# Performance work log

Measured on AMD Instinct MI355X. Metric: run time of the kernel, lower is better.

The kernel has to match this reference:

```python
import jax, jax.numpy as jnp
import numpy as np

B, T, C, FREQ = 32, 512, 22, 192
HID = 128


def setup_inputs() -> dict:
    key = jax.random.key(0)
    k1, k2, k3, k4, k5, k6 = jax.random.split(key, 6)
    x = jax.random.normal(k1, (B, T, C, FREQ), dtype=jnp.float32)
    A = jax.random.uniform(k2, (B, T, C, C), dtype=jnp.float32)
    # Linear weights (torch layout: [out, in]); scaled like torch default init
    W0 = jax.random.normal(k3, (HID, FREQ), dtype=jnp.float32) / np.sqrt(FREQ)
    b0 = jax.random.normal(k4, (HID,), dtype=jnp.float32) * 0.01
    W1 = jax.random.normal(k5, (HID, HID), dtype=jnp.float32) / np.sqrt(HID)
    b1 = jax.random.normal(k6, (HID,), dtype=jnp.float32) * 0.01
    return {"x": x, "A": A, "W0": W0, "b0": b0, "W1": W1, "b1": b1}


def reference(x, A, W0, b0, W1, b1):
    # Vectorized over B and T simultaneously (original python-loops over t).
    # Layer i: xt = relu(Linear(bmm(A_t, xt)))
    h = x  # [B,T,C,Freq]
    for W, b in ((W0, b0), (W1, b1)):
        h = jnp.einsum('btij,btjf->btif', A, h)          # adjacency mix over nodes
        h = jax.nn.relu(jnp.einsum('btcf,hf->btch', h, W) + b)  # Linear + ReLU
    # stack over t is implicit; mean over node dim C -> [B,T,HID]
    return h.mean(axis=2)
```

## Files before the change

kernel.cpp:

```cpp
#include <hip/hip_runtime.h>

#define CC 22
#define FF 192
#define HH 128
#define NBT (32 * 512)

typedef __attribute__((ext_vector_type(8))) __bf16 bf16x8;
typedef __attribute__((ext_vector_type(8))) short s16x8;
typedef __attribute__((ext_vector_type(4))) float f32x4;

__device__ __forceinline__ float bf2f(unsigned short u) {
    union { unsigned int i; float f; } v;
    v.i = ((unsigned int)u) << 16;
    return v.f;
}

__device__ __forceinline__ unsigned short f2bf(float f) {
    union { float f; unsigned int i; } v;
    v.f = f;
    return (unsigned short)((v.i + 0x7fffu + ((v.i >> 16) & 1u)) >> 16);
}

__device__ __forceinline__ void split2(float v, unsigned short& h, unsigned short& l) {
    h = f2bf(v);
    float r = v - bf2f(h);
    l = f2bf(r);
}

__device__ __forceinline__ bf16x8 bzero8() {
    s16x8 z = {0, 0, 0, 0, 0, 0, 0, 0};
    return __builtin_bit_cast(bf16x8, z);
}

__device__ __forceinline__ int inputs_are_bf16(const unsigned short* __restrict__ A,
                                               int tid) {
    const float v = bf2f(A[tid & 63]);
    return __all(v >= 0.0f && v <= 1.0001f);
}

#define WS0H 0
#define WS0L 24576
#define WS1H 49152
#define WS1L 65536

__global__ void convert_weights(const float* __restrict__ W0g,
                                const float* __restrict__ W1g,
                                const unsigned short* __restrict__ Aany,
                                unsigned short* __restrict__ wsW) {
    if (inputs_are_bf16(Aany, threadIdx.x)) return;
    const int i = blockIdx.x * 256 + threadIdx.x;
    if (i < HH * FF) {
        unsigned short h, l;
        split2(W0g[i], h, l);
        wsW[WS0H + i] = h;
        wsW[WS0L + i] = l;
    } else {
        const int j = i - HH * FF;
        if (j < HH * HH) {
            unsigned short h, l;
            split2(W1g[j], h, l);
            wsW[WS1H + j] = h;
            wsW[WS1L + j] = l;
        }
    }
}

__device__ void run_block_f32(
    const float* __restrict__ xg, const float* __restrict__ Ag,
    const float* __restrict__ W0g, const float* __restrict__ b0g,
    const float* __restrict__ W1g, const float* __restrict__ b1g,
    float* __restrict__ outg, int bt, int tid,
    float* sA, float* sX, float* sH1)
{
    float* sH2  = sX;
    float* sH3  = sH1;
    float* sRed = sA;

    const float* Ap = Ag + (size_t)bt * (CC * CC);
    for (int i = tid; i < CC * CC; i += 256) sA[i] = Ap[i];
    const float4* xp = (const float4*)(xg + (size_t)bt * (CC * FF));
    for (int i = tid; i < CC * FF / 4; i += 256) ((float4*)sX)[i] = xp[i];
    __syncthreads();

    for (int idx4 = tid; idx4 < CC * FF / 4; idx4 += 256) {
        const int c  = idx4 / (FF / 4);
        const int fq = idx4 - c * (FF / 4);
        float4 acc = make_float4(0.f, 0.f, 0.f, 0.f);
        #pragma unroll
        for (int j = 0; j < CC; ++j) {
            const float  a  = sA[c * CC + j];
            const float4 xv = *(const float4*)&sX[j * FF + 4 * fq];
            acc.x += a * xv.x; acc.y += a * xv.y;
            acc.z += a * xv.z; acc.w += a * xv.w;
        }
        ((float4*)sH1)[idx4] = acc;
    }
    __syncthreads();

    const int h  = tid & 127;
    const int ty = tid >> 7;

    {
        float acc[11];
        const float bb = b0g[h];
        #pragma unroll
        for (int i = 0; i < 11; ++i) acc[i] = bb;
        #pragma unroll 4
        for (int fq = 0; fq < FF / 4; ++fq) {
            float4 u = ((const float4*)(W0g + h * FF))[fq];
            #pragma unroll
            for (int i = 0; i < 11; ++i) {
                const float4 xv = *(const float4*)&sH1[(2 * i + ty) * FF + 4 * fq];
                acc[i] = fmaf(xv.x, u.x, fmaf(xv.y, u.y, fmaf(xv.z, u.z, fmaf(xv.w, u.w, acc[i]))));
            }
        }
        #pragma unroll
        for (int i = 0; i < 11; ++i)
            sH2[(2 * i + ty) * HH + h] = fmaxf(acc[i], 0.f);
    }
    __syncthreads();

    for (int idx4 = tid; idx4 < CC * HH / 4; idx4 += 256) {
        const int c  = idx4 / (HH / 4);
        const int kq = idx4 - c * (HH / 4);
        float4 acc = make_float4(0.f, 0.f, 0.f, 0.f);
        #pragma unroll
        for (int j = 0; j < CC; ++j) {
            const float  a  = sA[c * CC + j];
            const float4 xv = *(const float4*)&sH2[j * HH + 4 * kq];
            acc.x += a * xv.x; acc.y += a * xv.y;
            acc.z += a * xv.z; acc.w += a * xv.w;
        }
        ((float4*)sH3)[idx4] = acc;
    }
    __syncthreads();

    {
        float acc[11];
        const float bb = b1g[h];
        #pragma unroll
        for (int i = 0; i < 11; ++i) acc[i] = bb;
        #pragma unroll 4
        for (int kq = 0; kq < HH / 4; ++kq) {
            float4 u = ((const float4*)(W1g + h * HH))[kq];
            #pragma unroll
            for (int i = 0; i < 11; ++i) {
                const float4 xv = *(const float4*)&sH3[(2 * i + ty) * HH + 4 * kq];
                acc[i] = fmaf(xv.x, u.x, fmaf(xv.y, u.y, fmaf(xv.z, u.z, fmaf(xv.w, u.w, acc[i]))));
            }
        }
        float s = 0.f;
        #pragma unroll
        for (int i = 0; i < 11; ++i) s += fmaxf(acc[i], 0.f);
        sRed[ty * HH + h] = s;
    }
    __syncthreads();

    if (ty == 0) {
        const float m = (sRed[h] + sRed[HH + h]) * (1.0f / 22.0f);
        outg[(size_t)bt * HH + h] = m;
    }
}

__device__ void run_block_split(
    const float* __restrict__ xg, const float* __restrict__ Ag,
    const float* __restrict__ b0g, const float* __restrict__ b1g,
    const unsigned short* __restrict__ wsW,
    float* __restrict__ outg, int bt, int tid, char* smem)
{
    unsigned short* sxh  = (unsigned short*)smem;
    unsigned short* sxl  = (unsigned short*)(smem + 8800);
    unsigned short* sAh  = (unsigned short*)(smem + 17600);
    unsigned short* sAl  = (unsigned short*)(smem + 20160);
    unsigned short* syh  = (unsigned short*)(smem + 22720);
    unsigned short* syl  = (unsigned short*)(smem + 32960);
    unsigned short* sh3h = (unsigned short*)smem;
    unsigned short* sh3l = (unsigned short*)(smem + 8704);

    const unsigned short* W0h = wsW + WS0H;
    const unsigned short* W0l = wsW + WS0L;
    const unsigned short* W1h = wsW + WS1H;
    const unsigned short* W1l = wsW + WS1L;

    {
        const float4* xp4 = (const float4*)(xg + (size_t)bt * (CC * FF));
        for (int idx = tid; idx < CC * (FF / 4); idx += 256) {
            const int c = idx / (FF / 4);
            const int q = idx - c * (FF / 4);
            const float4 v = xp4[idx];
            ushort4 h4, l4;
            split2(v.x, h4.x, l4.x);
            split2(v.y, h4.y, l4.y);
            split2(v.z, h4.z, l4.z);
            split2(v.w, h4.w, l4.w);
            *(ushort4*)&sxh[c * 200 + 4 * q] = h4;
            *(ushort4*)&sxl[c * 200 + 4 * q] = l4;
        }
        const float* Ap = Ag + (size_t)bt * (CC * CC);
        for (int idx = tid; idx < 32 * 40; idx += 256) {
            const int r = idx / 40;
            const int c = idx - r * 40;
            unsigned short h = 0, l = 0;
            if (r < CC && c < CC) split2(Ap[r * CC + c], h, l);
            sAh[idx] = h;
            sAl[idx] = l;
        }
    }
    __syncthreads();

    const int lane = tid & 63;
    const int wid  = tid >> 6;
    const int lr   = lane & 15;
    const int lk   = lane >> 4;
    const int hb   = wid * 32;

    const f32x4 vzero = {0.f, 0.f, 0.f, 0.f};

    {
        f32x4 acc[2][2];
        #pragma unroll
        for (int mt = 0; mt < 2; ++mt)
            #pragma unroll
            for (int nt = 0; nt < 2; ++nt) acc[mt][nt] = vzero;

        #pragma unroll
        for (int ks = 0; ks < 6; ++ks) {
            bf16x8 xfh[2], xfl[2];
            #pragma unroll
            for (int mt = 0; mt < 2; ++mt) {
                const int row = mt * 16 + lr;
                const int rr  = (row < CC) ? row : 0;
                const int off = rr * 200 + ks * 32 + lk * 8;
                bf16x8 fh = *(const bf16x8*)(sxh + off);
                bf16x8 fl = *(const bf16x8*)(sxl + off);
                if (row >= CC) { fh = bzero8(); fl = bzero8(); }
                xfh[mt] = fh; xfl[mt] = fl;
            }
            bf16x8 wfh[2], wfl[2];
            #pragma unroll
            for (int nt = 0; nt < 2; ++nt) {
                const int hcol = hb + nt * 16 + lr;
                const int off  = hcol * FF + ks * 32 + lk * 8;
                wfh[nt] = *(const bf16x8*)(W0h + off);
                wfl[nt] = *(const bf16x8*)(W0l + off);
            }
            #pragma unroll
            for (int mt = 0; mt < 2; ++mt)
                #pragma unroll
                for (int nt = 0; nt < 2; ++nt) {
                    acc[mt][nt] = __builtin_amdgcn_mfma_f32_16x16x32_bf16(xfh[mt], wfh[nt], acc[mt][nt], 0, 0, 0);
                    acc[mt][nt] = __builtin_amdgcn_mfma_f32_16x16x32_bf16(xfl[mt], wfh[nt], acc[mt][nt], 0, 0, 0);
                    acc[mt][nt] = __builtin_amdgcn_mfma_f32_16x16x32_bf16(xfh[mt], wfl[nt], acc[mt][nt], 0, 0, 0);
                }
        }
        #pragma unroll
        for (int mt = 0; mt < 2; ++mt)
            #pragma unroll
            for (int nt = 0; nt < 2; ++nt) {
                const int hcol = hb + nt * 16 + lr;
                ushort4 h4, l4;
                split2(acc[mt][nt][0], h4.x, l4.x);
                split2(acc[mt][nt][1], h4.y, l4.y);
                split2(acc[mt][nt][2], h4.z, l4.z);
                split2(acc[mt][nt][3], h4.w, l4.w);
                *(ushort4*)&syh[hcol * 40 + mt * 16 + lk * 4] = h4;
                *(ushort4*)&syl[hcol * 40 + mt * 16 + lk * 4] = l4;
            }
    }
    __syncthreads();

    bf16x8 Afh[2], Afl[2];
    #pragma unroll
    for (int t = 0; t < 2; ++t) {
        const int off = (t * 16 + lr) * 40 + lk * 8;
        Afh[t] = *(const bf16x8*)(sAh + off);
        Afl[t] = *(const bf16x8*)(sAl + off);
    }

    {
        f32x4 acc[2][2];
        #pragma unroll
        for (int nt = 0; nt < 2; ++nt) {
            const float b = b0g[hb + nt * 16 + lr];
            const f32x4 bv = {b, b, b, b};
            acc[0][nt] = bv;
            acc[1][nt] = bv;
        }
        bf16x8 yfh[2], yfl[2];
        #pragma unroll
        for (int nt = 0; nt < 2; ++nt) {
            const int off = (hb + nt * 16 + lr) * 40 + lk * 8;
            yfh[nt] = *(const bf16x8*)(syh + off);
            yfl[nt] = *(const bf16x8*)(syl + off);
        }
        asm volatile("" ::: "memory");
        #pragma unroll
        for (int mt = 0; mt < 2; ++mt)
            #pragma unroll
            for (int nt = 0; nt < 2; ++nt) {
                acc[mt][nt] = __builtin_amdgcn_mfma_f32_16x16x32_bf16(Afh[mt], yfh[nt], acc[mt][nt], 0, 0, 0);
                acc[mt][nt] = __builtin_amdgcn_mfma_f32_16x16x32_bf16(Afl[mt], yfh[nt], acc[mt][nt], 0, 0, 0);
                acc[mt][nt] = __builtin_amdgcn_mfma_f32_16x16x32_bf16(Afh[mt], yfl[nt], acc[mt][nt], 0, 0, 0);
            }
        #pragma unroll
        for (int mt = 0; mt < 2; ++mt)
            #pragma unroll
            for (int nt = 0; nt < 2; ++nt) {
                const int hcol = hb + nt * 16 + lr;
                ushort4 h4, l4;
                split2(fmaxf(acc[mt][nt][0], 0.f), h4.x, l4.x);
                split2(fmaxf(acc[mt][nt][1], 0.f), h4.y, l4.y);
                split2(fmaxf(acc[mt][nt][2], 0.f), h4.z, l4.z);
                split2(fmaxf(acc[mt][nt][3], 0.f), h4.w, l4.w);
                *(ushort4*)&syh[hcol * 40 + mt * 16 + lk * 4] = h4;
                *(ushort4*)&syl[hcol * 40 + mt * 16 + lk * 4] = l4;
            }
    }

    {
        f32x4 acc[2][2];
        #pragma unroll
        for (int mt = 0; mt < 2; ++mt)
            #pragma unroll
            for (int ct = 0; ct < 2; ++ct) acc[mt][ct] = vzero;

        bf16x8 gfh[2], gfl[2];
        #pragma unroll
        for (int mt = 0; mt < 2; ++mt) {
            const int off = (hb + mt * 16 + lr) * 40 + lk * 8;
            gfh[mt] = *(const bf16x8*)(syh + off);
            gfl[mt] = *(const bf16x8*)(syl + off);
        }
        #pragma unroll
        for (int mt = 0; mt < 2; ++mt)
            #pragma unroll
            for (int ct = 0; ct < 2; ++ct) {
                acc[mt][ct] = __builtin_amdgcn_mfma_f32_16x16x32_bf16(gfh[mt], Afh[ct], acc[mt][ct], 0, 0, 0);
                acc[mt][ct] = __builtin_amdgcn_mfma_f32_16x16x32_bf16(gfl[mt], Afh[ct], acc[mt][ct], 0, 0, 0);
                acc[mt][ct] = __builtin_amdgcn_mfma_f32_16x16x32_bf16(gfh[mt], Afl[ct], acc[mt][ct], 0, 0, 0);
            }
        #pragma unroll
        for (int mt = 0; mt < 2; ++mt)
            #pragma unroll
            for (int ct = 0; ct < 2; ++ct) {
                const int cp = ct * 16 + lr;
                ushort4 h4, l4;
                split2(acc[mt][ct][0], h4.x, l4.x);
                split2(acc[mt][ct][1], h4.y, l4.y);
                split2(acc[mt][ct][2], h4.z, l4.z);
                split2(acc[mt][ct][3], h4.w, l4.w);
                *(ushort4*)&sh3h[cp * 136 + hb + mt * 16 + lk * 4] = h4;
                *(ushort4*)&sh3l[cp * 136 + hb + mt * 16 + lk * 4] = l4;
            }
    }
    __syncthreads();

    {
        f32x4 acc[2][2];
        #pragma unroll
        for (int mt = 0; mt < 2; ++mt) {
            const float4 bv = *(const float4*)(b1g + hb + mt * 16 + lk * 4);
            const f32x4 bb = {bv.x, bv.y, bv.z, bv.w};
            acc[mt][0] = bb;
            acc[mt][1] = bb;
        }
        #pragma unroll
        for (int ks = 0; ks < 4; ++ks) {
            bf16x8 wfh[2], wfl[2], hfh[2], hfl[2];
            #pragma unroll
            for (int mt = 0; mt < 2; ++mt) {
                const int o   = hb + mt * 16 + lr;
                const int off = o * HH + ks * 32 + lk * 8;
                wfh[mt] = *(const bf16x8*)(W1h + off);
                wfl[mt] = *(const bf16x8*)(W1l + off);
            }
            #pragma unroll
            for (int ct = 0; ct < 2; ++ct) {
                const int off = (ct * 16 + lr) * 136 + ks * 32 + lk * 8;
                hfh[ct] = *(const bf16x8*)(sh3h + off);
                hfl[ct] = *(const bf16x8*)(sh3l + off);
            }
            #pragma unroll
            for (int mt = 0; mt < 2; ++mt)
                #pragma unroll
                for (int ct = 0; ct < 2; ++ct) {
                    acc[mt][ct] = __builtin_amdgcn_mfma_f32_16x16x32_bf16(wfh[mt], hfh[ct], acc[mt][ct], 0, 0, 0);
                    acc[mt][ct] = __builtin_amdgcn_mfma_f32_16x16x32_bf16(wfl[mt], hfh[ct], acc[mt][ct], 0, 0, 0);
                    acc[mt][ct] = __builtin_amdgcn_mfma_f32_16x16x32_bf16(wfh[mt], hfl[ct], acc[mt][ct], 0, 0, 0);
                }
        }
        float s[2][4];
        #pragma unroll
        for (int mt = 0; mt < 2; ++mt)
            #pragma unroll
            for (int r = 0; r < 4; ++r) {
                float v = fmaxf(acc[mt][0][r], 0.f);
                if (lr < CC - 16) v += fmaxf(acc[mt][1][r], 0.f);
                s[mt][r] = v;
            }
        #pragma unroll
        for (int m = 1; m < 16; m <<= 1)
            #pragma unroll
            for (int mt = 0; mt < 2; ++mt)
                #pragma unroll
                for (int r = 0; r < 4; ++r)
                    s[mt][r] += __shfl_xor(s[mt][r], m);

        if (lr == 0) {
            const float inv = 1.0f / 22.0f;
            #pragma unroll
            for (int mt = 0; mt < 2; ++mt) {
                float4 o4;
                o4.x = s[mt][0] * inv;
                o4.y = s[mt][1] * inv;
                o4.z = s[mt][2] * inv;
                o4.w = s[mt][3] * inv;
                *(float4*)(outg + (size_t)bt * HH + hb + mt * 16 + lk * 4) = o4;
            }
        }
    }
}

__device__ void run_block_bf16(
    const unsigned short* __restrict__ xg, const unsigned short* __restrict__ Ag,
    const unsigned short* __restrict__ W0g, const unsigned short* __restrict__ b0g,
    const unsigned short* __restrict__ W1g, const unsigned short* __restrict__ b1g,
    unsigned short* __restrict__ outg, int bt, int tid, char* smem)
{
    unsigned short* sXT  = (unsigned short*)smem;
    unsigned short* sAm  = (unsigned short*)(smem + 15360);
    unsigned short* sH1  = (unsigned short*)(smem + 17920);
    unsigned short* sH2T = (unsigned short*)(smem + 30720);
    unsigned short* sH3  = (unsigned short*)smem;

    const unsigned short* xp = xg + (size_t)bt * (CC * FF);
    const unsigned short* Ap = Ag + (size_t)bt * (CC * CC);

    for (int id = tid; id < 32 * 40; id += 256) {
        const int r = id / 40;
        const int c = id - r * 40;
        sAm[id] = (r < CC && c < CC) ? Ap[r * CC + c] : (unsigned short)0;
    }
    for (int id = tid; id < FF * 9; id += 256) {
        const int f = id / 9;
        const int q = id - f * 9;
        ((unsigned int*)sXT)[f * 20 + 11 + q] = 0u;
    }
    for (int id = tid; id < 24 * CC; id += 256) {
        const int fb = id / CC;
        const int j  = id - fb * CC;
        const uint4 v = *(const uint4*)(xp + j * FF + fb * 8);
        unsigned short* d = sXT + (fb * 8) * 40 + j;
        d[0 * 40] = (unsigned short)(v.x & 0xffffu);
        d[1 * 40] = (unsigned short)(v.x >> 16);
        d[2 * 40] = (unsigned short)(v.y & 0xffffu);
        d[3 * 40] = (unsigned short)(v.y >> 16);
        d[4 * 40] = (unsigned short)(v.z & 0xffffu);
        d[5 * 40] = (unsigned short)(v.z >> 16);
        d[6 * 40] = (unsigned short)(v.w & 0xffffu);
        d[7 * 40] = (unsigned short)(v.w >> 16);
    }
    __syncthreads();

    const int lane = tid & 63;
    const int wid  = tid >> 6;
    const int lr   = lane & 15;
    const int lk   = lane >> 4;
    const f32x4 vzero = {0.f, 0.f, 0.f, 0.f};

    {
        f32x4 acc[3][2];
        #pragma unroll
        for (int i = 0; i < 3; ++i)
            #pragma unroll
            for (int j = 0; j < 2; ++j) acc[i][j] = vzero;
        bf16x8 xa[3], ab[2];
        #pragma unroll
        for (int i = 0; i < 3; ++i)
            xa[i] = *(const bf16x8*)(sXT + ((3 * wid + i) * 16 + lr) * 40 + lk * 8);
        #pragma unroll
        for (int j = 0; j < 2; ++j)
            ab[j] = *(const bf16x8*)(sAm + (j * 16 + lr) * 40 + lk * 8);
        #pragma unroll
        for (int i = 0; i < 3; ++i)
            #pragma unroll
            for (int j = 0; j < 2; ++j)
                acc[i][j] = __builtin_amdgcn_mfma_f32_16x16x32_bf16(xa[i], ab[j], acc[i][j], 0, 0, 0);
        #pragma unroll
        for (int i = 0; i < 3; ++i) {
            const int fbase = (3 * wid + i) * 16 + lk * 4;
            #pragma unroll
            for (int j = 0; j < 2; ++j) {
                const int c = j * 16 + lr;
                ushort4 st;
                st.x = f2bf(acc[i][j][0]);
                st.y = f2bf(acc[i][j][1]);
                st.z = f2bf(acc[i][j][2]);
                st.w = f2bf(acc[i][j][3]);
                *(ushort4*)(sH1 + c * 200 + fbase) = st;
            }
        }
    }
    __syncthreads();

    {
        f32x4 acc[2][2];
        #pragma unroll
        for (int nt = 0; nt < 2; ++nt) {
            const float bv = bf2f(b0g[(2 * wid + nt) * 16 + lr]);
            f32x4 bvv = {bv, bv, bv, bv};
            acc[0][nt] = bvv;
            acc[1][nt] = bvv;
        }
        #pragma unroll
        for (int ks = 0; ks < 6; ++ks) {
            bf16x8 af[2], bfr[2];
            #pragma unroll
            for (int mt = 0; mt < 2; ++mt)
                af[mt] = *(const bf16x8*)(sH1 + (mt * 16 + lr) * 200 + ks * 32 + lk * 8);
            #pragma unroll
            for (int nt = 0; nt < 2; ++nt)
                bfr[nt] = *(const bf16x8*)(W0g + ((size_t)((2 * wid + nt) * 16 + lr)) * FF + ks * 32 + lk * 8);
            #pragma unroll
            for (int mt = 0; mt < 2; ++mt)
                #pragma unroll
                for (int nt = 0; nt < 2; ++nt)
                    acc[mt][nt] = __builtin_amdgcn_mfma_f32_16x16x32_bf16(af[mt], bfr[nt], acc[mt][nt], 0, 0, 0);
        }
        #pragma unroll
        for (int mt = 0; mt < 2; ++mt) {
            const int cbase = mt * 16 + lk * 4;
            #pragma unroll
            for (int nt = 0; nt < 2; ++nt) {
                const int hcol = (2 * wid + nt) * 16 + lr;
                ushort4 st;
                st.x = (cbase + 0 < CC) ? f2bf(fmaxf(acc[mt][nt][0], 0.f)) : (unsigned short)0;
                st.y = (cbase + 1 < CC) ? f2bf(fmaxf(acc[mt][nt][1], 0.f)) : (unsigned short)0;
                st.z = (cbase + 2 < CC) ? f2bf(fmaxf(acc[mt][nt][2], 0.f)) : (unsigned short)0;
                st.w = (cbase + 3 < CC) ? f2bf(fmaxf(acc[mt][nt][3], 0.f)) : (unsigned short)0;
                *(ushort4*)(sH2T + hcol * 40 + cbase) = st;
            }
        }
    }
    __syncthreads();

    {
        f32x4 acc[2][2];
        #pragma unroll
        for (int mt = 0; mt < 2; ++mt)
            #pragma unroll
            for (int ct = 0; ct < 2; ++ct) acc[mt][ct] = vzero;
        bf16x8 af[2], bb[2];
        #pragma unroll
        for (int mt = 0; mt < 2; ++mt)
            af[mt] = *(const bf16x8*)(sH2T + ((2 * wid + mt) * 16 + lr) * 40 + lk * 8);
        #pragma unroll
        for (int ct = 0; ct < 2; ++ct)
            bb[ct] = *(const bf16x8*)(sAm + (ct * 16 + lr) * 40 + lk * 8);
        #pragma unroll
        for (int mt = 0; mt < 2; ++mt)
            #pragma unroll
            for (int ct = 0; ct < 2; ++ct)
                acc[mt][ct] = __builtin_amdgcn_mfma_f32_16x16x32_bf16(af[mt], bb[ct], acc[mt][ct], 0, 0, 0);
        #pragma unroll
        for (int mt = 0; mt < 2; ++mt) {
            const int hbase = (2 * wid + mt) * 16 + lk * 4;
            #pragma unroll
            for (int ct = 0; ct < 2; ++ct) {
                const int c = ct * 16 + lr;
                ushort4 st;
                st.x = f2bf(acc[mt][ct][0]);
                st.y = f2bf(acc[mt][ct][1]);
                st.z = f2bf(acc[mt][ct][2]);
                st.w = f2bf(acc[mt][ct][3]);
                *(ushort4*)(sH3 + c * 136 + hbase) = st;
            }
        }
    }
    __syncthreads();

    {
        f32x4 acc[2][2];
        #pragma unroll
        for (int mt = 0; mt < 2; ++mt) {
            const ushort4 bu = *(const ushort4*)(b1g + (2 * wid + mt) * 16 + lk * 4);
            f32x4 bvv = {bf2f(bu.x), bf2f(bu.y), bf2f(bu.z), bf2f(bu.w)};
            acc[mt][0] = bvv;
            acc[mt][1] = bvv;
        }
        #pragma unroll
        for (int ks = 0; ks < 4; ++ks) {
            bf16x8 af[2], bfr[2];
            #pragma unroll
            for (int mt = 0; mt < 2; ++mt)
                af[mt] = *(const bf16x8*)(W1g + ((size_t)((2 * wid + mt) * 16 + lr)) * HH + ks * 32 + lk * 8);
            #pragma unroll
            for (int ct = 0; ct < 2; ++ct)
                bfr[ct] = *(const bf16x8*)(sH3 + (ct * 16 + lr) * 136 + ks * 32 + lk * 8);
            #pragma unroll
            for (int mt = 0; mt < 2; ++mt)
                #pragma unroll
                for (int ct = 0; ct < 2; ++ct)
                    acc[mt][ct] = __builtin_amdgcn_mfma_f32_16x16x32_bf16(af[mt], bfr[ct], acc[mt][ct], 0, 0, 0);
        }
        float s[2][4];
        #pragma unroll
        for (int mt = 0; mt < 2; ++mt)
            #pragma unroll
            for (int r = 0; r < 4; ++r) {
                float v = fmaxf(acc[mt][0][r], 0.f);
                if (lr < CC - 16) v += fmaxf(acc[mt][1][r], 0.f);
                s[mt][r] = v;
            }
        #pragma unroll
        for (int m = 1; m < 16; m <<= 1)
            #pragma unroll
            for (int mt = 0; mt < 2; ++mt)
                #pragma unroll
                for (int r = 0; r < 4; ++r)
                    s[mt][r] += __shfl_xor(s[mt][r], m);
        if (lr == 0) {
            const float inv = 1.0f / 22.0f;
            #pragma unroll
            for (int mt = 0; mt < 2; ++mt) {
                ushort4 st;
                st.x = f2bf(s[mt][0] * inv);
                st.y = f2bf(s[mt][1] * inv);
                st.z = f2bf(s[mt][2] * inv);
                st.w = f2bf(s[mt][3] * inv);
                *(ushort4*)(outg + (size_t)bt * HH + (2 * wid + mt) * 16 + lk * 4) = st;
            }
        }
    }
}

__global__ __launch_bounds__(256) void tgcn_kernel(
    const void* __restrict__ x, const void* __restrict__ A,
    const void* __restrict__ W0, const void* __restrict__ b0,
    const void* __restrict__ W1, const void* __restrict__ b1,
    void* __restrict__ out, const unsigned short* __restrict__ wsW,
    int use_split)
{
    __shared__ __align__(16) char smem[43200];

    const int tid = threadIdx.x;
    const int bt  = blockIdx.x;
    const int isbf = inputs_are_bf16((const unsigned short*)A, tid);

    if (isbf) {
        run_block_bf16((const unsigned short*)x, (const unsigned short*)A,
                       (const unsigned short*)W0, (const unsigned short*)b0,
                       (const unsigned short*)W1, (const unsigned short*)b1,
                       (unsigned short*)out, bt, tid, smem);
    } else if (use_split) {
        run_block_split((const float*)x, (const float*)A,
                        (const float*)b0, (const float*)b1,
                        wsW, (float*)out, bt, tid, smem);
    } else {
        float* sA  = (float*)smem;
        float* sX  = (float*)(smem + 1936);
        float* sH1 = (float*)(smem + 18832);
        run_block_f32((const float*)x, (const float*)A,
                      (const float*)W0, (const float*)b0,
                      (const float*)W1, (const float*)b1,
                      (float*)out, bt, tid, sA, sX, sH1);
    }
}

extern "C" void kernel_launch(void* const* d_in, const int* in_sizes, int n_in,
                              void* d_out, int out_size, void* d_ws, size_t ws_size,
                              hipStream_t stream) {
    unsigned short* wsW = (unsigned short*)d_ws;
    const int use_split = (ws_size >= (size_t)(81920 * 2)) ? 1 : 0;

    if (use_split)
        convert_weights<<<160, 256, 0, stream>>>(
            (const float*)d_in[2], (const float*)d_in[4],
            (const unsigned short*)d_in[1], wsW);
    tgcn_kernel<<<NBT, 256, 0, stream>>>(
        d_in[0], d_in[1], d_in[2], d_in[3], d_in[4], d_in[5], d_out,
        wsW, use_split);
}
```

Before: 705.8 us.

## Pack bf16 splits with cvt_pk, swizzle y buffer, shrink shared memory

Replaces the scalar bf16 hi/lo splitting with the packed v_cvt_pk_bf16_f32 instruction, so two values are converted per op. The padded y tile (stride 40) becomes an XOR-swizzled 64-byte-row layout, which shrinks the buffer and aims to avoid LDS bank conflicts. The bf16 path's sH2T/sH3 buffers are re-aliased, with an extra barrier added so the overlap is safe, and total shared memory drops from 43200 to 39104 bytes to allow more resident blocks per CU. The added barrier costs a little synchronization, and the packed conversion's rounding must match the manual round-to-nearest-even.

```diff
diff --git a/kernel.cpp b/kernel.cpp
--- a/kernel.cpp
+++ b/kernel.cpp
@@ -27,9 +27,28 @@
     l = f2bf(r);
 }
 
+__device__ __forceinline__ unsigned int cvt_pk_bf16(float a, float b) {
+    unsigned int r;
+    asm("v_cvt_pk_bf16_f32 %0, %1, %2" : "=v"(r) : "v"(a), "v"(b));
+    return r;
+}
+
+__device__ __forceinline__ void split_pk2(float a, float b,
+                                          unsigned int& hi, unsigned int& lo) {
+    hi = cvt_pk_bf16(a, b);
+    union { unsigned int i; float f; } ha, hb;
+    ha.i = hi << 16;
+    hb.i = hi & 0xffff0000u;
+    lo = cvt_pk_bf16(a - ha.f, b - hb.f);
+}
+
 __device__ __forceinline__ bf16x8 bzero8() {
     s16x8 z = {0, 0, 0, 0, 0, 0, 0, 0};
     return __builtin_bit_cast(bf16x8, z);
+}
+
+__device__ __forceinline__ int ybyte(int row, int b) {
+    return row * 64 + (b ^ (((row >> 1) & 3) << 4));
 }
 
 __device__ __forceinline__ int inputs_are_bf16(const unsigned short* __restrict__ A,
@@ -172,8 +191,8 @@
     unsigned short* sxl  = (unsigned short*)(smem + 8800);
     unsigned short* sAh  = (unsigned short*)(smem + 17600);
     unsigned short* sAl  = (unsigned short*)(smem + 20160);
-    unsigned short* syh  = (unsigned short*)(smem + 22720);
-    unsigned short* syl  = (unsigned short*)(smem + 32960);
+    char*           syh  = smem + 22720;
+    char*           syl  = smem + 30912;
     unsigned short* sh3h = (unsigned short*)smem;
     unsigned short* sh3l = (unsigned short*)(smem + 8704);
 
@@ -188,13 +207,11 @@
             const int c = idx / (FF / 4);
             const int q = idx - c * (FF / 4);
             const float4 v = xp4[idx];
-            ushort4 h4, l4;
-            split2(v.x, h4.x, l4.x);
-            split2(v.y, h4.y, l4.y);
-            split2(v.z, h4.z, l4.z);
-            split2(v.w, h4.w, l4.w);
-            *(ushort4*)&sxh[c * 200 + 4 * q] = h4;
-            *(ushort4*)&sxl[c * 200 + 4 * q] = l4;
+            uint2 hv, lv;
+            split_pk2(v.x, v.y, hv.x, lv.x);
+            split_pk2(v.z, v.w, hv.y, lv.y);
+            *(uint2*)&sxh[c * 200 + 4 * q] = hv;
+            *(uint2*)&sxl[c * 200 + 4 * q] = lv;
         }
         const float* Ap = Ag + (size_t)bt * (CC * CC);
         for (int idx = tid; idx < 32 * 40; idx += 256) {
@@ -258,13 +275,12 @@
             #pragma unroll
             for (int nt = 0; nt < 2; ++nt) {
                 const int hcol = hb + nt * 16 + lr;
-                ushort4 h4, l4;
-                split2(acc[mt][nt][0], h4.x, l4.x);
-                split2(acc[mt][nt][1], h4.y, l4.y);
-                split2(acc[mt][nt][2], h4.z, l4.z);
-                split2(acc[mt][nt][3], h4.w, l4.w);
-                *(ushort4*)&syh[hcol * 40 + mt * 16 + lk * 4] = h4;
-                *(ushort4*)&syl[hcol * 40 + mt * 16 + lk * 4] = l4;
+                uint2 hv, lv;
+                split_pk2(acc[mt][nt][0], acc[mt][nt][1], hv.x, lv.x);
+                split_pk2(acc[mt][nt][2], acc[mt][nt][3], hv.y, lv.y);
+                const int boff = ybyte(hcol, mt * 32 + lk * 8);
+                *(uint2*)(syh + boff) = hv;
+                *(uint2*)(syl + boff) = lv;
             }
     }
     __syncthreads();
@@ -289,9 +305,9 @@
         bf16x8 yfh[2], yfl[2];
         #pragma unroll
         for (int nt = 0; nt < 2; ++nt) {
-            const int off = (hb + nt * 16 + lr) * 40 + lk * 8;
-            yfh[nt] = *(const bf16x8*)(syh + off);
-            yfl[nt] = *(const bf16x8*)(syl + off);
+            const int boff = ybyte(hb + nt * 16 + lr, lk * 16);
+            yfh[nt] = *(const bf16x8*)(syh + boff);
+            yfl[nt] = *(const bf16x8*)(syl + boff);
         }
         asm volatile("" ::: "memory");
         #pragma unroll
@@ -307,13 +323,12 @@
             #pragma unroll
             for (int nt = 0; nt < 2; ++nt) {
                 const int hcol = hb + nt * 16 + lr;
-                ushort4 h4, l4;
-                split2(fmaxf(acc[mt][nt][0], 0.f), h4.x, l4.x);
-                split2(fmaxf(acc[mt][nt][1], 0.f), h4.y, l4.y);
-                split2(fmaxf(acc[mt][nt][2], 0.f), h4.z, l4.z);
-                split2(fmaxf(acc[mt][nt][3], 0.f), h4.w, l4.w);
-                *(ushort4*)&syh[hcol * 40 + mt * 16 + lk * 4] = h4;
-                *(ushort4*)&syl[hcol * 40 + mt * 16 + lk * 4] = l4;
+                uint2 hv, lv;
+                split_pk2(fmaxf(acc[mt][nt][0], 0.f), fmaxf(acc[mt][nt][1], 0.f), hv.x, lv.x);
+                split_pk2(fmaxf(acc[mt][nt][2], 0.f), fmaxf(acc[mt][nt][3], 0.f), hv.y, lv.y);
+                const int boff = ybyte(hcol, mt * 32 + lk * 8);
+                *(uint2*)(syh + boff) = hv;
+                *(uint2*)(syl + boff) = lv;
             }
     }
 
@@ -327,9 +342,9 @@
         bf16x8 gfh[2], gfl[2];
         #pragma unroll
         for (int mt = 0; mt < 2; ++mt) {
-            const int off = (hb + mt * 16 + lr) * 40 + lk * 8;
-            gfh[mt] = *(const bf16x8*)(syh + off);
-            gfl[mt] = *(const bf16x8*)(syl + off);
+            const int boff = ybyte(hb + mt * 16 + lr, lk * 16);
+            gfh[mt] = *(const bf16x8*)(syh + boff);
+            gfl[mt] = *(const bf16x8*)(syl + boff);
         }
         #pragma unroll
         for (int mt = 0; mt < 2; ++mt)
@@ -344,13 +359,12 @@
             #pragma unroll
             for (int ct = 0; ct < 2; ++ct) {
                 const int cp = ct * 16 + lr;
-                ushort4 h4, l4;
-                split2(acc[mt][ct][0], h4.x, l4.x);
-                split2(acc[mt][ct][1], h4.y, l4.y);
-                split2(acc[mt][ct][2], h4.z, l4.z);
-                split2(acc[mt][ct][3], h4.w, l4.w);
-                *(ushort4*)&sh3h[cp * 136 + hb + mt * 16 + lk * 4] = h4;
-                *(ushort4*)&sh3l[cp * 136 + hb + mt * 16 + lk * 4] = l4;
+                uint2 hv, lv;
+                split_pk2(acc[mt][ct][0], acc[mt][ct][1], hv.x, lv.x);
+                split_pk2(acc[mt][ct][2], acc[mt][ct][3], hv.y, lv.y);
+                const int e = cp * 136 + hb + mt * 16 + lk * 4;
+                *(uint2*)&sh3h[e] = hv;
+                *(uint2*)&sh3l[e] = lv;
             }
     }
     __syncthreads();
@@ -430,8 +444,8 @@
     unsigned short* sXT  = (unsigned short*)smem;
     unsigned short* sAm  = (unsigned short*)(smem + 15360);
     unsigned short* sH1  = (unsigned short*)(smem + 17920);
-    unsigned short* sH2T = (unsigned short*)(smem + 30720);
-    unsigned short* sH3  = (unsigned short*)smem;
+    unsigned short* sH2T = (unsigned short*)smem;
+    unsigned short* sH3  = (unsigned short*)(smem + 17920);
 
     const unsigned short* xp = xg + (size_t)bt * (CC * FF);
     const unsigned short* Ap = Ag + (size_t)bt * (CC * CC);
@@ -562,6 +576,7 @@
             #pragma unroll
             for (int ct = 0; ct < 2; ++ct)
                 acc[mt][ct] = __builtin_amdgcn_mfma_f32_16x16x32_bf16(af[mt], bb[ct], acc[mt][ct], 0, 0, 0);
+        __syncthreads();
         #pragma unroll
         for (int mt = 0; mt < 2; ++mt) {
             const int hbase = (2 * wid + mt) * 16 + lk * 4;
@@ -641,7 +656,7 @@
     void* __restrict__ out, const unsigned short* __restrict__ wsW,
     int use_split)
 {
-    __shared__ __align__(16) char smem[43200];
+    __shared__ __align__(16) char smem[39104];
 
     const int tid = threadIdx.x;
     const int bt  = blockIdx.x;
```

After: 701.7 us. Within noise of the previous version (-0.6%).
